# Kernel tuning notes

Measured on AMD Instinct MI355X. Metric: run time of the kernel, lower is better.

Reference implementation:

```python
import jax, jax.numpy as jnp
import numpy as np

H, D = 16, 1024
HD = D // H  # 64

def setup_inputs() -> dict:
    key = jax.random.key(0)
    ks = jax.random.split(key, 11)
    B, S = 2, 2048
    s_in = 1.0 / np.sqrt(D)
    return {
        "V": jax.random.normal(ks[0], (B, S, D), jnp.float32),
        "K": jax.random.normal(ks[1], (B, S, D), jnp.float32),
        "Q": jax.random.normal(ks[2], (B, S, D), jnp.float32),
        # stacked per-head Linear weights, torch layout [out,in] -> [H, HD, D]
        "Wv": jax.random.normal(ks[3], (H, HD, D), jnp.float32) * s_in,
        "bv": jnp.zeros((H, HD), jnp.float32),
        "Wk": jax.random.normal(ks[4], (H, HD, D), jnp.float32) * s_in,
        "bk": jnp.zeros((H, HD), jnp.float32),
        "Wq": jax.random.normal(ks[5], (H, HD, D), jnp.float32) * s_in,
        "bq": jnp.zeros((H, HD), jnp.float32),
        "Wo": jax.random.normal(ks[6], (D, D), jnp.float32) * s_in,
        "bo": jnp.zeros((D,), jnp.float32),
    }

def reference(V, K, Q, Wv, bv, Wk, bk, Wq, bq, Wo, bo):
    scale = HD ** (-0.5)
    # per-head projections fused into one batched GEMM: [B,S,D] x [H,HD,D] -> [B,H,S,HD]
    q = jnp.einsum('bsd,hed->bhse', Q, Wq) + bq[None, :, None, :]
    k = jnp.einsum('bsd,hed->bhse', K, Wk) + bk[None, :, None, :]
    v = jnp.einsum('bsd,hed->bhse', V, Wv) + bv[None, :, None, :]
    # scaled dot-product attention
    scores = jnp.einsum('bhqe,bhke->bhqk', q, k) * scale  # [B,H,S,S]
    p = jax.nn.softmax(scores, axis=-1)
    att = jnp.einsum('bhqk,bhke->bhqe', p, v)  # [B,H,S,HD]
    # concat heads (head 0 first, matching the torch cat order) then output proj
    B, _, S, _ = att.shape
    cat = jnp.transpose(att, (0, 2, 1, 3)).reshape(B, S, H * HD)
    return cat @ Wo.T + bo
```

## Files before the change

### kernel.cpp

```cpp
#include <hip/hip_runtime.h>
#include <cstdint>
#include <cstddef>

typedef __bf16 bf16_t;
typedef bf16_t bf16x8 __attribute__((ext_vector_type(8)));
typedef bf16_t bf16x4 __attribute__((ext_vector_type(4)));
typedef float f32x4 __attribute__((ext_vector_type(4)));
typedef float f32x2 __attribute__((ext_vector_type(2)));

__device__ __forceinline__ void gl_lds16(const void* g, void* l) {
  __builtin_amdgcn_global_load_lds(
      (const __attribute__((address_space(1))) void*)g,
      (__attribute__((address_space(3))) void*)l, 16, 0, 0);
}

__device__ __forceinline__ f32x4 mfma16(bf16x8 a, bf16x8 b, f32x4 c) {
  return __builtin_amdgcn_mfma_f32_16x16x32_bf16(a, b, c, 0, 0, 0);
}

__device__ __forceinline__ float exp2_fast(float x) {
  float r;
  asm("v_exp_f32 %0, %1" : "=v"(r) : "v"(x));
  return r;
}

#define SCHED_FENCE() __builtin_amdgcn_sched_barrier(0)
#define WAIT_VM0()   do { asm volatile("s_waitcnt vmcnt(0)");   SCHED_FENCE(); } while (0)
#define WAIT_LGKM0() do { asm volatile("s_waitcnt lgkmcnt(0)"); SCHED_FENCE(); } while (0)
#define RAW_BAR()    do { __builtin_amdgcn_s_barrier();         SCHED_FENCE(); } while (0)

struct CvtArgs { const float* src[7]; bf16_t* dst[7]; };

__global__ __launch_bounds__(256) void convert_all(CvtArgs a) {
  unsigned g = blockIdx.x * 256u + threadIdx.x;
  unsigned seg, off;
  if (g < 524288u) {
    seg = g >> 17; off = g & 131071u;
  } else {
    unsigned h = g - 524288u;
    seg = 4u + (h >> 19); off = h & 524287u;
  }
  const float4* s = (const float4*)a.src[seg] + (size_t)off * 2;
  float4 x0 = s[0], x1 = s[1];
  bf16x8 o;
  o[0] = (bf16_t)x0.x; o[1] = (bf16_t)x0.y; o[2] = (bf16_t)x0.z; o[3] = (bf16_t)x0.w;
  o[4] = (bf16_t)x1.x; o[5] = (bf16_t)x1.y; o[6] = (bf16_t)x1.z; o[7] = (bf16_t)x1.w;
  *(bf16x8*)(a.dst[seg] + (size_t)off * 8) = o;
}

__device__ __forceinline__ void stage128(const bf16_t* src, bf16_t* dst, int t, int w) {
  #pragma unroll
  for (int i = 0; i < 4; i++) {
    int g = t + i * 256;
    int r = g >> 3, pc = g & 7;
    int lc = pc ^ (r & 7);
    gl_lds16(src + (size_t)r * 1024 + lc * 8, dst + i * 2048 + w * 512);
  }
}
__device__ __forceinline__ void stage128x32(const bf16_t* src, bf16_t* dst, int t, int w) {
  #pragma unroll
  for (int i = 0; i < 2; i++) {
    int g = t + i * 256;
    int rp = g >> 3, pc = g & 7;
    int lc = pc ^ (rp & 7);
    int R = rp * 2 + (lc >> 2), c4 = lc & 3;
    gl_lds16(src + (size_t)R * 1024 + c4 * 8, dst + i * 2048 + w * 512);
  }
}
__device__ __forceinline__ void stage64x32(const bf16_t* src, bf16_t* dst, int t, int w) {
  int g = t;
  int rp = g >> 3, pc = g & 7;
  int lc = pc ^ (rp & 7);
  int R = rp * 2 + (lc >> 2), c4 = lc & 3;
  gl_lds16(src + (size_t)R * 1024 + c4 * 8, dst + w * 512);
}
__device__ __forceinline__ bf16x8 frag32(const bf16_t* buf, int R, int lq) {
  int rp = R >> 1;
  int pc = ((R & 1) * 4 + lq) ^ (rp & 7);
  return *(const bf16x8*)(buf + rp * 64 + pc * 8);
}

struct ProjArgs {
  const bf16_t* A[3]; const bf16_t* W[3]; const float* bias[3];
  bf16_t* out[3]; float scale[3];
};

__global__ __launch_bounds__(256, 3) void gemm_proj(ProjArgs p) {
  __shared__ __attribute__((aligned(16))) unsigned char smem[49152];
  const int z = blockIdx.z;
  const bf16_t* A = p.A[z] + (size_t)blockIdx.x * 128 * 1024;
  const bf16_t* W = p.W[z] + (size_t)blockIdx.y * 128 * 1024;

  const int t = threadIdx.x;
  const int w = t >> 6, l = t & 63;
  const int lq = l >> 4, lr = l & 15;
  const int mq = w & 1, nq = w >> 1;

  f32x4 acc[4][4];
  f32x4 zero = {0.f, 0.f, 0.f, 0.f};
  #pragma unroll
  for (int i = 0; i < 4; i++)
    #pragma unroll
    for (int j = 0; j < 4; j++) acc[i][j] = zero;

  stage128x32(A,      (bf16_t*)smem,                t, w);
  stage128x32(W,      (bf16_t*)(smem + 8192),       t, w);
  stage128x32(A + 32, (bf16_t*)(smem + 16384),      t, w);
  stage128x32(W + 32, (bf16_t*)(smem + 16384 + 8192), t, w);
  asm volatile("s_waitcnt vmcnt(4)");
  SCHED_FENCE();
  RAW_BAR();

#define PROJ_STEP(KT, BUF, NBUF, DOSTAGE, WAITN)                                 \
  {                                                                              \
    bf16_t* as = (bf16_t*)(smem + (BUF) * 16384);                                \
    bf16_t* bs = (bf16_t*)(smem + (BUF) * 16384 + 8192);                         \
    if (DOSTAGE) {                                                               \
      bf16_t* an = (bf16_t*)(smem + (NBUF) * 16384);                             \
      stage128x32(A + ((KT) + 2) * 32, an, t, w);                                \
      stage128x32(W + ((KT) + 2) * 32, an + 4096, t, w);                         \
    }                                                                            \
    SCHED_FENCE();                                                               \
    bf16x8 af[4], bfr[4];                                                        \
    _Pragma("unroll")                                                            \
    for (int i = 0; i < 4; i++) af[i] = frag32(as, mq * 64 + i * 16 + lr, lq);   \
    _Pragma("unroll")                                                            \
    for (int j = 0; j < 4; j++) bfr[j] = frag32(bs, nq * 64 + j * 16 + lr, lq);  \
    __builtin_amdgcn_s_setprio(1);                                               \
    _Pragma("unroll")                                                            \
    for (int i = 0; i < 4; i++)                                                  \
      _Pragma("unroll")                                                          \
      for (int j = 0; j < 4; j++)                                                \
        acc[i][j] = mfma16(af[i], bfr[j], acc[i][j]);                            \
    __builtin_amdgcn_s_setprio(0);                                               \
    asm volatile("s_waitcnt vmcnt(" WAITN ") lgkmcnt(0)");                       \
    SCHED_FENCE();                                                               \
    RAW_BAR();                                                                   \
  }

  for (int k3 = 0; k3 < 30; k3 += 3) {
    PROJ_STEP(k3 + 0, 0, 2, true, "4");
    PROJ_STEP(k3 + 1, 1, 0, true, "4");
    PROJ_STEP(k3 + 2, 2, 1, true, "4");
  }
  PROJ_STEP(30, 0, 2, false, "0");
  PROJ_STEP(31, 1, 0, false, "0");
#undef PROJ_STEP

  const float* bias = p.bias[z];
  const float scale = p.scale[z];
  __syncthreads();
  bf16_t* ts = (bf16_t*)smem;
  #pragma unroll
  for (int i = 0; i < 4; i++) {
    #pragma unroll
    for (int j = 0; j < 4; j++) {
      int nl = nq * 64 + j * 16 + lr;
      float bz = bias[blockIdx.y * 128 + nl];
      #pragma unroll
      for (int r = 0; r < 4; r++) {
        int ml = mq * 64 + i * 16 + lq * 4 + r;
        bf16_t val = (bf16_t)((acc[i][j][r] + bz) * scale);
        if (z == 0) {
          int mlp = (ml & 96) | (((ml >> 2) & 3) << 3) | (((ml >> 4) & 1) << 2) | (ml & 3);
          ts[nl * 136 + mlp] = val;
        } else {
          ts[ml * 136 + nl] = val;
        }
      }
    }
  }
  __syncthreads();
  bf16_t* out = p.out[z];
  const int b = blockIdx.x >> 4, sbase = (blockIdx.x & 15) * 128;
  if (z == 0) {
    #pragma unroll
    for (int ii = 0; ii < 8; ii++) {
      int idx = t * 8 + ii * 2048;
      int rr = idx >> 7, cc = idx & 127;
      int n = blockIdx.y * 128 + rr;
      int h = n >> 6, e = n & 63;
      bf16x8 vq = *(const bf16x8*)(ts + rr * 136 + cc);
      *(bf16x8*)(out + ((size_t)(b * 16 + h) * 64 + e) * 2048 + sbase + cc) = vq;
    }
  } else {
    #pragma unroll
    for (int ii = 0; ii < 8; ii++) {
      int idx = t * 8 + ii * 2048;
      int rr = idx >> 7, cc = idx & 127;
      int n = blockIdx.y * 128 + cc;
      int h = n >> 6, e = n & 63;
      bf16x8 vq = *(const bf16x8*)(ts + rr * 136 + cc);
      *(bf16x8*)(out + ((size_t)(b * 16 + h) * 2048 + sbase + rr) * 64 + e) = vq;
    }
  }
}

__global__ __launch_bounds__(256, 2) void attn(
    const bf16_t* __restrict__ qw, const bf16_t* __restrict__ kw,
    const bf16_t* __restrict__ vtw, bf16_t* __restrict__ att)
{
  __shared__ __attribute__((aligned(16))) unsigned char smem[49152];
  const int bh = blockIdx.x, qt = blockIdx.y;
  const int t = threadIdx.x, w = t >> 6, l = t & 63, lq = l >> 4, lr = l & 15;

  const bf16_t* kb0 = kw + (size_t)bh * 131072;
  const bf16_t* vb0 = vtw + (size_t)bh * 131072;
  bf16_t* qstage = (bf16_t*)(smem + 32768);

  const bf16_t* qbase = qw + ((size_t)bh * 2048 + qt * 128) * 64;
  #pragma unroll
  for (int i = 0; i < 4; i++) {
    int g = t + i * 256;
    int r = g >> 3, pc = g & 7;
    int lc = pc ^ (r & 7);
    gl_lds16(qbase + (size_t)r * 64 + lc * 8, qstage + i * 2048 + w * 512);
  }
  #pragma unroll
  for (int tt = 0; tt < 2; tt++) {
    bf16_t* kn = (bf16_t*)(smem + tt * 16384);
    const bf16_t* kbase = kb0 + (size_t)tt * 4096;
    const bf16_t* vbase = vb0 + (size_t)tt * 64;
    #pragma unroll
    for (int i = 0; i < 2; i++) {
      int g = t + i * 256;
      int r = g >> 3, pc = g & 7;
      int lc = pc ^ (r & 7);
      gl_lds16(kbase + (size_t)r * 64 + lc * 8, kn + i * 2048 + w * 512);
      gl_lds16(vbase + (size_t)r * 2048 + lc * 8, kn + 4096 + i * 2048 + w * 512);
    }
  }
  asm volatile("s_waitcnt vmcnt(8)");
  SCHED_FENCE();
  RAW_BAR();
  bf16x8 qf[2][2];
  #pragma unroll
  for (int gq = 0; gq < 2; gq++)
    #pragma unroll
    for (int kk = 0; kk < 2; kk++) {
      int R = w * 32 + gq * 16 + lr;
      int ch = (kk * 4 + lq) ^ (R & 7);
      qf[gq][kk] = *(const bf16x8*)(qstage + R * 64 + ch * 8);
    }
  asm volatile("s_waitcnt vmcnt(4) lgkmcnt(0)");
  SCHED_FENCE();
  RAW_BAR();

  f32x4 O[2][4];
  f32x4 zero = {0.f, 0.f, 0.f, 0.f};
  #pragma unroll
  for (int gq = 0; gq < 2; gq++)
    #pragma unroll
    for (int et = 0; et < 4; et++) O[gq][et] = zero;
  f32x2 lsv[2];
  lsv[0] = f32x2{0.f, 0.f}; lsv[1] = f32x2{0.f, 0.f};
  bf16x8 vfA[8], vfB[8];
  bf16x8 pbA[2][2], pbB[2][2];

#define ATTN_BODY(KT, BUF, NBUF, PBOUT, PBIN, VFOUT, VFIN, FIRST, DOSTAGE, ENDWAIT) \
  {                                                                              \
    bf16_t* ksb = (bf16_t*)(smem + (BUF) * 16384);                               \
    bf16_t* vsb = (bf16_t*)(smem + (BUF) * 16384 + 8192);                        \
    if (DOSTAGE) {                                                               \
      bf16_t* kn = (bf16_t*)(smem + (NBUF) * 16384);                             \
      const bf16_t* kbase = kb0 + (size_t)((KT) + 2) * 4096;                     \
      const bf16_t* vbase = vb0 + (size_t)((KT) + 2) * 64;                       \
      _Pragma("unroll")                                                          \
      for (int i = 0; i < 2; i++) {                                              \
        int g = t + i * 256;                                                     \
        int r = g >> 3, pc = g & 7;                                              \
        int lc = pc ^ (r & 7);                                                   \
        gl_lds16(kbase + (size_t)r * 64 + lc * 8, kn + i * 2048 + w * 512);      \
        gl_lds16(vbase + (size_t)r * 2048 + lc * 8, kn + 4096 + i * 2048 + w * 512); \
      }                                                                          \
    }                                                                            \
    SCHED_FENCE();                                                               \
    f32x4 sc[2][4];                                                              \
    _Pragma("unroll")                                                            \
    for (int gq = 0; gq < 2; gq++)                                               \
      _Pragma("unroll")                                                          \
      for (int j = 0; j < 4; j++) sc[gq][j] = zero;                              \
    __builtin_amdgcn_s_setprio(1);                                               \
    if (!(FIRST)) {                                                              \
      _Pragma("unroll")                                                          \
      for (int ks2 = 0; ks2 < 2; ks2++)                                          \
        _Pragma("unroll")                                                        \
        for (int et = 0; et < 4; et++) {                                         \
          O[0][et] = mfma16((VFIN)[ks2 * 4 + et], (PBIN)[0][ks2], O[0][et]);     \
          O[1][et] = mfma16((VFIN)[ks2 * 4 + et], (PBIN)[1][ks2], O[1][et]);     \
        }                                                                        \
    }                                                                            \
    _Pragma("unroll")                                                            \
    for (int kk = 0; kk < 2; kk++)                                               \
      _Pragma("unroll")                                                          \
      for (int j = 0; j < 4; j++) {                                              \
        int R = j * 16 + lr;                                                     \
        int ch = (kk * 4 + lq) ^ (R & 7);                                        \
        bf16x8 kf = *(const bf16x8*)(ksb + R * 64 + ch * 8);                     \
        sc[0][j] = mfma16(kf, qf[0][kk], sc[0][j]);                              \
        sc[1][j] = mfma16(kf, qf[1][kk], sc[1][j]);                              \
      }                                                                          \
    __builtin_amdgcn_s_setprio(0);                                               \
    _Pragma("unroll")                                                            \
    for (int ks2 = 0; ks2 < 2; ks2++)                                            \
      _Pragma("unroll")                                                          \
      for (int et = 0; et < 4; et++) {                                           \
        int R = et * 16 + lr;                                                    \
        int ch = (ks2 * 4 + lq) ^ (R & 7);                                       \
        (VFOUT)[ks2 * 4 + et] = *(const bf16x8*)(vsb + R * 64 + ch * 8);         \
      }                                                                          \
    _Pragma("unroll")                                                            \
    for (int gq = 0; gq < 2; gq++)                                               \
      _Pragma("unroll")                                                          \
      for (int ks2 = 0; ks2 < 2; ks2++)                                          \
        _Pragma("unroll")                                                        \
        for (int r = 0; r < 4; r++) {                                            \
          float e0 = exp2_fast(sc[gq][2 * ks2][r]);                              \
          float e1 = exp2_fast(sc[gq][2 * ks2 + 1][r]);                          \
          f32x2 ee = {e0, e1};                                                   \
          lsv[gq] += ee;                                                         \
          (PBOUT)[gq][ks2][r] = (bf16_t)e0;                                      \
          (PBOUT)[gq][ks2][4 + r] = (bf16_t)e1;                                  \
        }                                                                        \
          \
          \
    asm volatile("s_waitcnt vmcnt(" ENDWAIT ") lgkmcnt(0)");                     \
    SCHED_FENCE();                                                               \
    RAW_BAR();                                                                   \
  }

  ATTN_BODY(0, 0, 2, pbA, pbB, vfA, vfB, true,  true, "4");
  ATTN_BODY(1, 1, 0, pbB, pbA, vfB, vfA, false, true, "4");
  ATTN_BODY(2, 2, 1, pbA, pbB, vfA, vfB, false, true, "4");
  ATTN_BODY(3, 0, 2, pbB, pbA, vfB, vfA, false, true, "4");
  ATTN_BODY(4, 1, 0, pbA, pbB, vfA, vfB, false, true, "4");
  ATTN_BODY(5, 2, 1, pbB, pbA, vfB, vfA, false, true, "4");
  for (int g6 = 6; g6 < 30; g6 += 6) {
    ATTN_BODY(g6 + 0, 0, 2, pbA, pbB, vfA, vfB, false, true, "4");
    ATTN_BODY(g6 + 1, 1, 0, pbB, pbA, vfB, vfA, false, true, "4");
    ATTN_BODY(g6 + 2, 2, 1, pbA, pbB, vfA, vfB, false, true, "4");
    ATTN_BODY(g6 + 3, 0, 2, pbB, pbA, vfB, vfA, false, true, "4");
    ATTN_BODY(g6 + 4, 1, 0, pbA, pbB, vfA, vfB, false, true, "4");
    ATTN_BODY(g6 + 5, 2, 1, pbB, pbA, vfB, vfA, false, true, "4");
  }
  ATTN_BODY(30, 0, 2, pbA, pbB, vfA, vfB, false, false, "0");
  ATTN_BODY(31, 1, 0, pbB, pbA, vfB, vfA, false, false, "0");
#undef ATTN_BODY

  #pragma unroll
  for (int ks2 = 0; ks2 < 2; ks2++)
    #pragma unroll
    for (int et = 0; et < 4; et++) {
      O[0][et] = mfma16(vfB[ks2 * 4 + et], pbB[0][ks2], O[0][et]);
      O[1][et] = mfma16(vfB[ks2 * 4 + et], pbB[1][ks2], O[1][et]);
    }

  float s0 = lsv[0][0] + lsv[0][1];
  float s1 = lsv[1][0] + lsv[1][1];
  s0 += __shfl_xor(s0, 16);
  s0 += __shfl_xor(s0, 32);
  s1 += __shfl_xor(s1, 16);
  s1 += __shfl_xor(s1, 32);
  float rinv[2] = {1.0f / s0, 1.0f / s1};

  bf16_t* ts = (bf16_t*)smem;
  #pragma unroll
  for (int gq = 0; gq < 2; gq++)
    #pragma unroll
    for (int et = 0; et < 4; et++) {
      bf16x4 pv;
      #pragma unroll
      for (int r = 0; r < 4; r++) pv[r] = (bf16_t)(O[gq][et][r] * rinv[gq]);
      *(bf16x4*)(ts + (w * 32 + gq * 16 + lr) * 72 + et * 16 + lq * 4) = pv;
    }
  __syncthreads();
  const int b = bh >> 4, h = bh & 15;
  #pragma unroll
  for (int i = 0; i < 4; i++) {
    int c = t + i * 256;
    int row = c >> 3, c8 = c & 7;
    bf16x8 vv = *(const bf16x8*)(ts + row * 72 + c8 * 8);
    *(bf16x8*)(att + ((size_t)b * 2048 + qt * 128 + row) * 1024 + h * 64 + c8 * 8) = vv;
  }
}

__global__ __launch_bounds__(256, 2) void gemm_out(
    const bf16_t* __restrict__ A, const bf16_t* __restrict__ W,
    const float* __restrict__ bias, float* __restrict__ out)
{
  __shared__ __attribute__((aligned(16))) unsigned char smem[36864];
  const bf16_t* Ab = A + (size_t)blockIdx.x * 64 * 1024;
  const bf16_t* Wb = W + (size_t)blockIdx.y * 128 * 1024;
  const int t = threadIdx.x, w = t >> 6, l = t & 63, lq = l >> 4, lr = l & 15;
  const int mh = w & 1, nh = w >> 1;

  f32x4 acc[2][4];
  f32x4 zero = {0.f, 0.f, 0.f, 0.f};
  #pragma unroll
  for (int i = 0; i < 2; i++)
    #pragma unroll
    for (int j = 0; j < 4; j++) acc[i][j] = zero;

  stage64x32 (Ab,      (bf16_t*)smem,                 t, w);
  stage128x32(Wb,      (bf16_t*)(smem + 4096),        t, w);
  stage64x32 (Ab + 32, (bf16_t*)(smem + 12288),       t, w);
  stage128x32(Wb + 32, (bf16_t*)(smem + 12288 + 4096), t, w);
  asm volatile("s_waitcnt vmcnt(3)");
  SCHED_FENCE();
  RAW_BAR();

#define OUT_STEP(KT, BUF, NBUF, DOSTAGE, WAITN)                                  \
  {                                                                              \
    bf16_t* as = (bf16_t*)(smem + (BUF) * 12288);                                \
    bf16_t* bs = (bf16_t*)(smem + (BUF) * 12288 + 4096);                         \
    if (DOSTAGE) {                                                               \
      bf16_t* an = (bf16_t*)(smem + (NBUF) * 12288);                             \
      stage64x32 (Ab + ((KT) + 2) * 32, an, t, w);                               \
      stage128x32(Wb + ((KT) + 2) * 32, an + 2048, t, w);                        \
    }                                                                            \
    SCHED_FENCE();                                                               \
    bf16x8 af[2], bfr[4];                                                        \
    _Pragma("unroll")                                                            \
    for (int i = 0; i < 2; i++) af[i] = frag32(as, mh * 32 + i * 16 + lr, lq);   \
    _Pragma("unroll")                                                            \
    for (int j = 0; j < 4; j++) bfr[j] = frag32(bs, nh * 64 + j * 16 + lr, lq);  \
    __builtin_amdgcn_s_setprio(1);                                               \
    _Pragma("unroll")                                                            \
    for (int i = 0; i < 2; i++)                                                  \
      _Pragma("unroll")                                                          \
      for (int j = 0; j < 4; j++)                                                \
        acc[i][j] = mfma16(af[i], bfr[j], acc[i][j]);                            \
    __builtin_amdgcn_s_setprio(0);                                               \
    asm volatile("s_waitcnt vmcnt(" WAITN ") lgkmcnt(0)");                       \
    SCHED_FENCE();                                                               \
    RAW_BAR();                                                                   \
  }

  for (int k3 = 0; k3 < 30; k3 += 3) {
    OUT_STEP(k3 + 0, 0, 2, true, "3");
    OUT_STEP(k3 + 1, 1, 0, true, "3");
    OUT_STEP(k3 + 2, 2, 1, true, "3");
  }
  OUT_STEP(30, 0, 2, false, "0");
  OUT_STEP(31, 1, 0, false, "0");
#undef OUT_STEP

  #pragma unroll
  for (int i = 0; i < 2; i++) {
    #pragma unroll
    for (int j = 0; j < 4; j++) {
      int col = blockIdx.y * 128 + nh * 64 + j * 16 + lr;
      float bz = bias[col];
      #pragma unroll
      for (int r = 0; r < 4; r++) {
        int row = blockIdx.x * 64 + mh * 32 + i * 16 + lq * 4 + r;
        out[(size_t)row * 1024 + col] = acc[i][j][r] + bz;
      }
    }
  }
}

extern "C" void kernel_launch(void* const* d_in, const int* in_sizes, int n_in,
                              void* d_out, int out_size, void* d_ws, size_t ws_size,
                              hipStream_t stream) {
  (void)in_sizes; (void)n_in; (void)out_size;
  const float* V  = (const float*)d_in[0];
  const float* Kx = (const float*)d_in[1];
  const float* Q  = (const float*)d_in[2];
  const float* Wv = (const float*)d_in[3];
  const float* bv = (const float*)d_in[4];
  const float* Wk = (const float*)d_in[5];
  const float* bk = (const float*)d_in[6];
  const float* Wq = (const float*)d_in[7];
  const float* bq = (const float*)d_in[8];
  const float* Wo = (const float*)d_in[9];
  const float* bo = (const float*)d_in[10];

  const size_t E = 1048576;
  if (ws_size < 20 * E * sizeof(bf16_t)) return;

  bf16_t* ws = (bf16_t*)d_ws;
  bf16_t* cWo   = ws;
  bf16_t* cWv   = ws + E;
  bf16_t* cWk   = ws + 2 * E;
  bf16_t* cWq   = ws + 3 * E;
  bf16_t* q_ws  = ws + 4 * E;
  bf16_t* k_ws  = ws + 8 * E;
  bf16_t* vt_ws = ws + 12 * E;
  bf16_t* att_ws= ws + 16 * E;

  bf16_t* cV = att_ws;
  bf16_t* cK = (bf16_t*)d_out;
  bf16_t* cQ = (bf16_t*)d_out + 4 * E;

  CvtArgs ca;
  ca.src[0] = Wo; ca.src[1] = Wv; ca.src[2] = Wk; ca.src[3] = Wq;
  ca.src[4] = V;  ca.src[5] = Kx; ca.src[6] = Q;
  ca.dst[0] = cWo; ca.dst[1] = cWv; ca.dst[2] = cWk; ca.dst[3] = cWq;
  ca.dst[4] = cV;  ca.dst[5] = cK;  ca.dst[6] = cQ;
  convert_all<<<8192, 256, 0, stream>>>(ca);

  ProjArgs pa;
  pa.A[0] = cV;  pa.A[1] = cK;  pa.A[2] = cQ;
  pa.W[0] = cWv; pa.W[1] = cWk; pa.W[2] = cWq;
  pa.bias[0] = bv; pa.bias[1] = bk; pa.bias[2] = bq;
  pa.out[0] = vt_ws; pa.out[1] = k_ws; pa.out[2] = q_ws;
  pa.scale[0] = 1.f; pa.scale[1] = 1.f; pa.scale[2] = 0.125f * 1.4426950408889634f;
  gemm_proj<<<dim3(32, 8, 3), 256, 0, stream>>>(pa);

  attn<<<dim3(32, 16), 256, 0, stream>>>(q_ws, k_ws, vt_ws, att_ws);

  gemm_out<<<dim3(64, 8), 256, 0, stream>>>(att_ws, cWo, bo, (float*)d_out);
}
```

Before: 201.4 us.

## Restructure attention K/V pipeline into two-tile double-buffered steps with fewer barriers

Replaces the triple-buffered per-tile pipeline, which had one barrier per 64-key tile, with a double-buffered loop. Each step loads two K/V tiles at once and processes both before a single barrier, halving barrier count. LDS use grows from 48KB to 64KB, which could cut occupancy below the two blocks per CU requested by launch bounds. The wait is now vmcnt(0), so prefetch depth is reduced and load latency may be exposed at each step.

Result: no change. 202.6 us (+0.6%).

```diff
diff --git a/kernel.cpp b/kernel.cpp
--- a/kernel.cpp
+++ b/kernel.cpp
@@ -200,7 +200,7 @@
     const bf16_t* __restrict__ qw, const bf16_t* __restrict__ kw,
     const bf16_t* __restrict__ vtw, bf16_t* __restrict__ att)
 {
-  __shared__ __attribute__((aligned(16))) unsigned char smem[49152];
+  __shared__ __attribute__((aligned(16))) unsigned char smem[65536];
   const int bh = blockIdx.x, qt = blockIdx.y;
   const int t = threadIdx.x, w = t >> 6, l = t & 63, lq = l >> 4, lr = l & 15;
 
@@ -242,7 +242,7 @@
       int ch = (kk * 4 + lq) ^ (R & 7);
       qf[gq][kk] = *(const bf16x8*)(qstage + R * 64 + ch * 8);
     }
-  asm volatile("s_waitcnt vmcnt(4) lgkmcnt(0)");
+  asm volatile("s_waitcnt vmcnt(0) lgkmcnt(0)");
   SCHED_FENCE();
   RAW_BAR();
 
@@ -257,31 +257,15 @@
   bf16x8 vfA[8], vfB[8];
   bf16x8 pbA[2][2], pbB[2][2];
 
-#define ATTN_BODY(KT, BUF, NBUF, PBOUT, PBIN, VFOUT, VFIN, FIRST, DOSTAGE, ENDWAIT) \
+#define SUBSTEP(KSB, VSB, VFOUT, PBOUT, VFIN, PBIN, DOPV)                        \
   {                                                                              \
-    bf16_t* ksb = (bf16_t*)(smem + (BUF) * 16384);                               \
-    bf16_t* vsb = (bf16_t*)(smem + (BUF) * 16384 + 8192);                        \
-    if (DOSTAGE) {                                                               \
-      bf16_t* kn = (bf16_t*)(smem + (NBUF) * 16384);                             \
-      const bf16_t* kbase = kb0 + (size_t)((KT) + 2) * 4096;                     \
-      const bf16_t* vbase = vb0 + (size_t)((KT) + 2) * 64;                       \
-      _Pragma("unroll")                                                          \
-      for (int i = 0; i < 2; i++) {                                              \
-        int g = t + i * 256;                                                     \
-        int r = g >> 3, pc = g & 7;                                              \
-        int lc = pc ^ (r & 7);                                                   \
-        gl_lds16(kbase + (size_t)r * 64 + lc * 8, kn + i * 2048 + w * 512);      \
-        gl_lds16(vbase + (size_t)r * 2048 + lc * 8, kn + 4096 + i * 2048 + w * 512); \
-      }                                                                          \
-    }                                                                            \
-    SCHED_FENCE();                                                               \
     f32x4 sc[2][4];                                                              \
     _Pragma("unroll")                                                            \
     for (int gq = 0; gq < 2; gq++)                                               \
       _Pragma("unroll")                                                          \
       for (int j = 0; j < 4; j++) sc[gq][j] = zero;                              \
     __builtin_amdgcn_s_setprio(1);                                               \
-    if (!(FIRST)) {                                                              \
+    if (DOPV) {                                                                  \
       _Pragma("unroll")                                                          \
       for (int ks2 = 0; ks2 < 2; ks2++)                                          \
         _Pragma("unroll")                                                        \
@@ -296,7 +280,7 @@
       for (int j = 0; j < 4; j++) {                                              \
         int R = j * 16 + lr;                                                     \
         int ch = (kk * 4 + lq) ^ (R & 7);                                        \
-        bf16x8 kf = *(const bf16x8*)(ksb + R * 64 + ch * 8);                     \
+        bf16x8 kf = *(const bf16x8*)((KSB) + R * 64 + ch * 8);                   \
         sc[0][j] = mfma16(kf, qf[0][kk], sc[0][j]);                              \
         sc[1][j] = mfma16(kf, qf[1][kk], sc[1][j]);                              \
       }                                                                          \
@@ -307,7 +291,7 @@
       for (int et = 0; et < 4; et++) {                                           \
         int R = et * 16 + lr;                                                    \
         int ch = (ks2 * 4 + lq) ^ (R & 7);                                       \
-        (VFOUT)[ks2 * 4 + et] = *(const bf16x8*)(vsb + R * 64 + ch * 8);         \
+        (VFOUT)[ks2 * 4 + et] = *(const bf16x8*)((VSB) + R * 64 + ch * 8);       \
       }                                                                          \
     _Pragma("unroll")                                                            \
     for (int gq = 0; gq < 2; gq++)                                               \
@@ -322,30 +306,37 @@
           (PBOUT)[gq][ks2][r] = (bf16_t)e0;                                      \
           (PBOUT)[gq][ks2][4 + r] = (bf16_t)e1;                                  \
         }                                                                        \
-          \
-          \
-    asm volatile("s_waitcnt vmcnt(" ENDWAIT ") lgkmcnt(0)");                     \
-    SCHED_FENCE();                                                               \
-    RAW_BAR();                                                                   \
-  }
-
-  ATTN_BODY(0, 0, 2, pbA, pbB, vfA, vfB, true,  true, "4");
-  ATTN_BODY(1, 1, 0, pbB, pbA, vfB, vfA, false, true, "4");
-  ATTN_BODY(2, 2, 1, pbA, pbB, vfA, vfB, false, true, "4");
-  ATTN_BODY(3, 0, 2, pbB, pbA, vfB, vfA, false, true, "4");
-  ATTN_BODY(4, 1, 0, pbA, pbB, vfA, vfB, false, true, "4");
-  ATTN_BODY(5, 2, 1, pbB, pbA, vfB, vfA, false, true, "4");
-  for (int g6 = 6; g6 < 30; g6 += 6) {
-    ATTN_BODY(g6 + 0, 0, 2, pbA, pbB, vfA, vfB, false, true, "4");
-    ATTN_BODY(g6 + 1, 1, 0, pbB, pbA, vfB, vfA, false, true, "4");
-    ATTN_BODY(g6 + 2, 2, 1, pbA, pbB, vfA, vfB, false, true, "4");
-    ATTN_BODY(g6 + 3, 0, 2, pbB, pbA, vfB, vfA, false, true, "4");
-    ATTN_BODY(g6 + 4, 1, 0, pbA, pbB, vfA, vfB, false, true, "4");
-    ATTN_BODY(g6 + 5, 2, 1, pbB, pbA, vfB, vfA, false, true, "4");
-  }
-  ATTN_BODY(30, 0, 2, pbA, pbB, vfA, vfB, false, false, "0");
-  ATTN_BODY(31, 1, 0, pbB, pbA, vfB, vfA, false, false, "0");
-#undef ATTN_BODY
+  }
+
+  for (int i = 0; i < 16; ++i) {
+    const int cur = (i & 1) << 15;
+    const int oth = cur ^ 32768;
+    if (i < 15) {
+      const bf16_t* kb2 = kb0 + (size_t)(2 * i + 2) * 4096;
+      const bf16_t* vb2 = vb0 + (size_t)(2 * i + 2) * 64;
+      const bf16_t* kb3 = kb2 + 4096;
+      const bf16_t* vb3 = vb2 + 64;
+      #pragma unroll
+      for (int ii = 0; ii < 2; ii++) {
+        int g = t + ii * 256;
+        int r = g >> 3, pc = g & 7;
+        int lc = pc ^ (r & 7);
+        bf16_t* d0 = (bf16_t*)(smem + oth) + ii * 2048 + w * 512;
+        gl_lds16(kb2 + (size_t)r * 64 + lc * 8, d0);
+        gl_lds16(vb2 + (size_t)r * 2048 + lc * 8, d0 + 4096);
+        gl_lds16(kb3 + (size_t)r * 64 + lc * 8, d0 + 8192);
+        gl_lds16(vb3 + (size_t)r * 2048 + lc * 8, d0 + 12288);
+      }
+    }
+    SCHED_FENCE();
+    bf16_t* base = (bf16_t*)(smem + cur);
+    SUBSTEP(base, base + 4096, vfA, pbA, vfB, pbB, (i > 0))
+    SUBSTEP(base + 8192, base + 12288, vfB, pbB, vfA, pbA, true)
+    asm volatile("s_waitcnt vmcnt(0) lgkmcnt(0)");
+    SCHED_FENCE();
+    RAW_BAR();
+  }
+#undef SUBSTEP
 
   #pragma unroll
   for (int ks2 = 0; ks2 < 2; ks2++)
```
